# Kernel tuning notes

Measured on AMD Instinct MI355X. Metric: run time of the kernel, lower is better.

## Reference

```python
import jax, jax.numpy as jnp
import numpy as np

ALPHA = 0.2  # LeakyReLU negative slope


def setup_inputs() -> dict:
    key = jax.random.key(0)
    k1, k2, k3 = jax.random.split(key, 3)
    B, N, IN, OUT = 64, 2048, 1024, 1024
    features = jax.random.normal(k1, (B, N, IN), dtype=jnp.float32)
    # Xavier-uniform-ish scaling for weights
    W = jax.random.normal(k2, (OUT, IN), dtype=jnp.float32) * (1.0 / np.sqrt(IN))
    w_b = jnp.zeros((OUT,), dtype=jnp.float32)
    a_w = jax.random.normal(k3, (2 * OUT,), dtype=jnp.float32) * (1.0 / np.sqrt(2 * OUT))
    a_b = jnp.zeros((), dtype=jnp.float32)
    bias_out = jnp.zeros((OUT,), dtype=jnp.float32)
    return {"features": features, "W": W, "w_b": w_b, "a_w": a_w, "a_b": a_b, "bias_out": bias_out}


def reference(features, W, w_b, a_w, a_b, bias_out):
    # h = Linear(in_dim, out_dim)(features): [B, N, D]
    h = jnp.einsum('bni,di->bnd', features, W) + w_b
    D = h.shape[-1]
    a1, a2 = a_w[:D], a_w[D:]
    # concat([h_expand, h]) @ a == h[:, :1] . a1 + h . a2  (h_expand broadcasts node 0)
    e = (h[:, 0:1, :] @ a1[:, None]) + jnp.einsum('bnd,d->bn', h, a2)[..., None] + a_b  # [B, N, 1]
    e = jnp.where(e >= 0, e, ALPHA * e)  # LeakyReLU
    attention = jax.nn.softmax(e, axis=1)  # softmax over nodes, [B, N, 1]
    # dropout p=0.0 -> identity
    pooled = jnp.einsum('bnk,bnd->bkd', attention, h)  # [B, 1, D]
    return jax.nn.relu(pooled + bias_out)
```

## Files before the change

kernel.cpp:

```cpp
#include <hip/hip_runtime.h>

#define ALPHA 0.2f
constexpr int B_   = 64;
constexpr int N_   = 2048;
constexpr int IN_  = 1024;
constexpr int OUT_ = 1024;
constexpr int CHUNK = 256;
constexpr int NCH   = N_ / CHUNK;
constexpr int RPW   = CHUNK / 4;

constexpr size_t WA2   = 0;
constexpr size_t E0P   = 1024;
constexpr size_t ZPART = 5120;
constexpr size_t GPART = 8192;
constexpr size_t GV    = 532480;

__device__ inline float wave_reduce_sum(float v) {
    #pragma unroll
    for (int off = 32; off > 0; off >>= 1) v += __shfl_xor(v, off);
    return v;
}

__global__ void kPre(const float* __restrict__ W, const float* __restrict__ f,
                     const float* __restrict__ wb, const float* __restrict__ aw,
                     float* __restrict__ ws) {
    int s = blockIdx.x;
    int t = threadIdx.x;
    int c  = t & 15;
    int rg = t >> 4;
    int col = s * 16 + c;
    float a1acc = 0.f, a2acc = 0.f;
    for (int i = 0; i < 64; ++i) {
        int d = rg * 64 + i;
        float w = W[(size_t)d * IN_ + col];
        a1acc += aw[d] * w;
        a2acc += aw[OUT_ + d] * w;
    }
    __shared__ float s1[16][16], s2[16][16];
    __shared__ float wa1L[16];
    __shared__ float wbshare_s;
    s1[rg][c] = a1acc;
    s2[rg][c] = a2acc;
    __syncthreads();
    if (t < 16) {
        float x1 = 0.f, x2 = 0.f;
        #pragma unroll
        for (int r = 0; r < 16; ++r) { x1 += s1[r][t]; x2 += s2[r][t]; }
        wa1L[t] = x1;
        ws[WA2 + s * 16 + t] = x2;
    }
    if (t == 0) {
        float x = 0.f;
        #pragma unroll
        for (int c2 = 0; c2 < 16; ++c2) {
            int cc = s * 16 + c2;
            x += wb[cc] * (aw[cc] + aw[OUT_ + cc]);
        }
        wbshare_s = x;
    }
    __syncthreads();
    int b = t >> 2, q = t & 3;
    float4 fv = ((const float4*)(f + (size_t)b * N_ * IN_ + s * 16))[q];
    float4 w1 = ((const float4*)wa1L)[q];
    float dotv = fv.x * w1.x + fv.y * w1.y + fv.z * w1.z + fv.w * w1.w;
    dotv += __shfl_xor(dotv, 1);
    dotv += __shfl_xor(dotv, 2);
    if (q == 0) ws[E0P + s * 64 + b] = dotv + wbshare_s;
}

__global__ void kMain(const float* __restrict__ f, const float* __restrict__ ab,
                      float* __restrict__ ws) {
    int b = blockIdx.y, chunk = blockIdx.x;
    int t = threadIdx.x, wave = t >> 6, lane = t & 63;

    __shared__ float cstS;
    if (t < 64) {
        float v = ws[E0P + (size_t)t * 64 + b];
        v = wave_reduce_sum(v);
        if (t == 0) cstS = v + ab[0];
    }
    __syncthreads();
    float cst = cstS;

    const float4* wa2_4 = (const float4*)(ws + WA2);
    float4 ra2[4];
    #pragma unroll
    for (int k = 0; k < 4; ++k) ra2[k] = wa2_4[k * 64 + lane];

    const float4* fbase = (const float4*)(f + ((size_t)b * N_ + (size_t)chunk * CHUNK) * IN_);
    float4 acc[4];
    #pragma unroll
    for (int k = 0; k < 4; ++k) acc[k] = make_float4(0.f, 0.f, 0.f, 0.f);
    float z = 0.f;

    float4 v[4], nv[4];
    int r = wave;
    #pragma unroll
    for (int k = 0; k < 4; ++k) v[k] = fbase[(size_t)r * 256 + k * 64 + lane];

    for (int i = 0; i < RPW; ++i) {
        int rn = r + 4;
        if (i + 1 < RPW) {
            #pragma unroll
            for (int k = 0; k < 4; ++k) nv[k] = fbase[(size_t)rn * 256 + k * 64 + lane];
        }
        float dot = 0.f;
        #pragma unroll
        for (int k = 0; k < 4; ++k)
            dot += v[k].x * ra2[k].x + v[k].y * ra2[k].y + v[k].z * ra2[k].z + v[k].w * ra2[k].w;
        dot = wave_reduce_sum(dot);
        float e = dot + cst;
        e = e >= 0.f ? e : ALPHA * e;
        float w = __expf(e);
        z += w;
        #pragma unroll
        for (int k = 0; k < 4; ++k) {
            acc[k].x += w * v[k].x; acc[k].y += w * v[k].y;
            acc[k].z += w * v[k].z; acc[k].w += w * v[k].w;
        }
        if (i + 1 < RPW) {
            #pragma unroll
            for (int k = 0; k < 4; ++k) v[k] = nv[k];
        }
        r = rn;
    }

    __shared__ float4 gbuf[4][256];
    __shared__ float  zbuf[4];
    #pragma unroll
    for (int k = 0; k < 4; ++k) gbuf[wave][k * 64 + lane] = acc[k];
    if (lane == 0) zbuf[wave] = z;
    __syncthreads();
    float4 s0 = gbuf[0][t], s1 = gbuf[1][t], s2 = gbuf[2][t], s3 = gbuf[3][t];
    float4 s = make_float4(s0.x + s1.x + s2.x + s3.x, s0.y + s1.y + s2.y + s3.y,
                           s0.z + s1.z + s2.z + s3.z, s0.w + s1.w + s2.w + s3.w);
    ((float4*)(ws + GPART))[((size_t)b * NCH + chunk) * 256 + t] = s;
    if (t == 0) ws[ZPART + b * NCH + chunk] = zbuf[0] + zbuf[1] + zbuf[2] + zbuf[3];
}

__global__ void kE(float* __restrict__ ws) {
    int b = blockIdx.x, t = threadIdx.x;
    __shared__ float zinv;
    if (t == 0) {
        float zz = 0.f;
        #pragma unroll
        for (int c = 0; c < NCH; ++c) zz += ws[ZPART + b * NCH + c];
        zinv = 1.0f / zz;
    }
    __syncthreads();
    const float4* gp = (const float4*)(ws + GPART);
    float4 acc = make_float4(0.f, 0.f, 0.f, 0.f);
    #pragma unroll
    for (int c = 0; c < NCH; ++c) {
        float4 v = gp[((size_t)b * NCH + c) * 256 + t];
        acc.x += v.x; acc.y += v.y; acc.z += v.z; acc.w += v.w;
    }
    acc.x *= zinv; acc.y *= zinv; acc.z *= zinv; acc.w *= zinv;
    ((float4*)(ws + GV))[b * 256 + t] = acc;
}

__global__ void kF(const float* __restrict__ W, const float* __restrict__ wb,
                   const float* __restrict__ bias, const float* __restrict__ ws,
                   float* __restrict__ out) {
    int t = threadIdx.x, wave = t >> 6, lane = t & 63;
    int d  = blockIdx.x * 4 + wave;
    int b0 = blockIdx.y * 32;
    const float4* w4 = (const float4*)(W + (size_t)d * IN_);
    float4 wreg[4];
    #pragma unroll
    for (int k = 0; k < 4; ++k) wreg[k] = w4[k * 64 + lane];
    float wbb = wb[d] + bias[d];
    const float4* gv = (const float4*)(ws + GV);
    #pragma unroll 4
    for (int bi = 0; bi < 32; ++bi) {
        int b = b0 + bi;
        float acc = 0.f;
        #pragma unroll
        for (int k = 0; k < 4; ++k) {
            float4 g = gv[b * 256 + k * 64 + lane];
            acc += g.x * wreg[k].x + g.y * wreg[k].y + g.z * wreg[k].z + g.w * wreg[k].w;
        }
        acc = wave_reduce_sum(acc);
        if (lane == 0) {
            float p = acc + wbb;
            out[(size_t)b * OUT_ + d] = p > 0.f ? p : 0.f;
        }
    }
}

extern "C" void kernel_launch(void* const* d_in, const int* in_sizes, int n_in,
                              void* d_out, int out_size, void* d_ws, size_t ws_size,
                              hipStream_t stream) {
    const float* f    = (const float*)d_in[0];
    const float* W    = (const float*)d_in[1];
    const float* wb   = (const float*)d_in[2];
    const float* aw   = (const float*)d_in[3];
    const float* ab   = (const float*)d_in[4];
    const float* bias = (const float*)d_in[5];
    float* out = (float*)d_out;
    float* ws  = (float*)d_ws;

    kPre <<<dim3(64), 256, 0, stream>>>(W, f, wb, aw, ws);
    kMain<<<dim3(NCH, B_), 256, 0, stream>>>(f, ab, ws);
    kE   <<<dim3(B_), 256, 0, stream>>>(ws);
    kF   <<<dim3(OUT_ / 4, 2), 256, 0, stream>>>(W, wb, bias, ws, out);
}
```

Before: 122.3 us.

## Fuse four kernels into one cooperative kernel with grid-wide syncs

Merges the precompute, main attention-pooling, reduction and output projection kernels into a single cooperative kernel of 512 blocks separated by grid.sync barriers. This is meant to remove the launch overhead and inter-kernel gaps of four separate launches. In exchange the grid is fixed at 512 blocks and depends on all of them being co-resident, and each grid.sync adds its own barrier cost. Several phases also leave most blocks idle.

```diff
diff --git a/kernel.cpp b/kernel.cpp
--- a/kernel.cpp
+++ b/kernel.cpp
@@ -1,4 +1,7 @@
 #include <hip/hip_runtime.h>
+#include <hip/hip_cooperative_groups.h>
+
+namespace cg = cooperative_groups;
 
 #define ALPHA 0.2f
 constexpr int B_   = 64;
@@ -8,6 +11,7 @@
 constexpr int CHUNK = 256;
 constexpr int NCH   = N_ / CHUNK;
 constexpr int RPW   = CHUNK / 4;
+constexpr int GRID  = 512;
 
 constexpr size_t WA2   = 0;
 constexpr size_t E0P   = 1024;
@@ -21,169 +25,176 @@
     return v;
 }
 
-__global__ void kPre(const float* __restrict__ W, const float* __restrict__ f,
-                     const float* __restrict__ wb, const float* __restrict__ aw,
-                     float* __restrict__ ws) {
-    int s = blockIdx.x;
-    int t = threadIdx.x;
-    int c  = t & 15;
-    int rg = t >> 4;
-    int col = s * 16 + c;
-    float a1acc = 0.f, a2acc = 0.f;
-    for (int i = 0; i < 64; ++i) {
-        int d = rg * 64 + i;
-        float w = W[(size_t)d * IN_ + col];
-        a1acc += aw[d] * w;
-        a2acc += aw[OUT_ + d] * w;
-    }
-    __shared__ float s1[16][16], s2[16][16];
-    __shared__ float wa1L[16];
-    __shared__ float wbshare_s;
-    s1[rg][c] = a1acc;
-    s2[rg][c] = a2acc;
-    __syncthreads();
-    if (t < 16) {
-        float x1 = 0.f, x2 = 0.f;
-        #pragma unroll
-        for (int r = 0; r < 16; ++r) { x1 += s1[r][t]; x2 += s2[r][t]; }
-        wa1L[t] = x1;
-        ws[WA2 + s * 16 + t] = x2;
-    }
-    if (t == 0) {
-        float x = 0.f;
-        #pragma unroll
-        for (int c2 = 0; c2 < 16; ++c2) {
-            int cc = s * 16 + c2;
-            x += wb[cc] * (aw[cc] + aw[OUT_ + cc]);
-        }
-        wbshare_s = x;
-    }
-    __syncthreads();
-    int b = t >> 2, q = t & 3;
-    float4 fv = ((const float4*)(f + (size_t)b * N_ * IN_ + s * 16))[q];
-    float4 w1 = ((const float4*)wa1L)[q];
-    float dotv = fv.x * w1.x + fv.y * w1.y + fv.z * w1.z + fv.w * w1.w;
-    dotv += __shfl_xor(dotv, 1);
-    dotv += __shfl_xor(dotv, 2);
-    if (q == 0) ws[E0P + s * 64 + b] = dotv + wbshare_s;
-}
-
-__global__ void kMain(const float* __restrict__ f, const float* __restrict__ ab,
-                      float* __restrict__ ws) {
-    int b = blockIdx.y, chunk = blockIdx.x;
-    int t = threadIdx.x, wave = t >> 6, lane = t & 63;
-
-    __shared__ float cstS;
-    if (t < 64) {
-        float v = ws[E0P + (size_t)t * 64 + b];
-        v = wave_reduce_sum(v);
-        if (t == 0) cstS = v + ab[0];
-    }
-    __syncthreads();
-    float cst = cstS;
-
-    const float4* wa2_4 = (const float4*)(ws + WA2);
-    float4 ra2[4];
-    #pragma unroll
-    for (int k = 0; k < 4; ++k) ra2[k] = wa2_4[k * 64 + lane];
-
-    const float4* fbase = (const float4*)(f + ((size_t)b * N_ + (size_t)chunk * CHUNK) * IN_);
-    float4 acc[4];
-    #pragma unroll
-    for (int k = 0; k < 4; ++k) acc[k] = make_float4(0.f, 0.f, 0.f, 0.f);
-    float z = 0.f;
-
-    float4 v[4], nv[4];
-    int r = wave;
-    #pragma unroll
-    for (int k = 0; k < 4; ++k) v[k] = fbase[(size_t)r * 256 + k * 64 + lane];
-
-    for (int i = 0; i < RPW; ++i) {
-        int rn = r + 4;
-        if (i + 1 < RPW) {
-            #pragma unroll
-            for (int k = 0; k < 4; ++k) nv[k] = fbase[(size_t)rn * 256 + k * 64 + lane];
-        }
-        float dot = 0.f;
-        #pragma unroll
-        for (int k = 0; k < 4; ++k)
-            dot += v[k].x * ra2[k].x + v[k].y * ra2[k].y + v[k].z * ra2[k].z + v[k].w * ra2[k].w;
-        dot = wave_reduce_sum(dot);
-        float e = dot + cst;
-        e = e >= 0.f ? e : ALPHA * e;
-        float w = __expf(e);
-        z += w;
-        #pragma unroll
-        for (int k = 0; k < 4; ++k) {
-            acc[k].x += w * v[k].x; acc[k].y += w * v[k].y;
-            acc[k].z += w * v[k].z; acc[k].w += w * v[k].w;
-        }
-        if (i + 1 < RPW) {
-            #pragma unroll
-            for (int k = 0; k < 4; ++k) v[k] = nv[k];
-        }
-        r = rn;
-    }
+__global__ void __launch_bounds__(256, 2)
+kAll(const float* __restrict__ W, const float* __restrict__ f,
+     const float* __restrict__ wb, const float* __restrict__ aw,
+     const float* __restrict__ ab, const float* __restrict__ bias,
+     float* __restrict__ out, float* __restrict__ ws) {
+    cg::grid_group grid = cg::this_grid();
+    const int bid = blockIdx.x;
+    const int t = threadIdx.x;
+    const int wave = t >> 6, lane = t & 63;
 
     __shared__ float4 gbuf[4][256];
     __shared__ float  zbuf[4];
-    #pragma unroll
-    for (int k = 0; k < 4; ++k) gbuf[wave][k * 64 + lane] = acc[k];
-    if (lane == 0) zbuf[wave] = z;
-    __syncthreads();
-    float4 s0 = gbuf[0][t], s1 = gbuf[1][t], s2 = gbuf[2][t], s3 = gbuf[3][t];
-    float4 s = make_float4(s0.x + s1.x + s2.x + s3.x, s0.y + s1.y + s2.y + s3.y,
-                           s0.z + s1.z + s2.z + s3.z, s0.w + s1.w + s2.w + s3.w);
-    ((float4*)(ws + GPART))[((size_t)b * NCH + chunk) * 256 + t] = s;
-    if (t == 0) ws[ZPART + b * NCH + chunk] = zbuf[0] + zbuf[1] + zbuf[2] + zbuf[3];
-}
-
-__global__ void kE(float* __restrict__ ws) {
-    int b = blockIdx.x, t = threadIdx.x;
-    __shared__ float zinv;
-    if (t == 0) {
-        float zz = 0.f;
-        #pragma unroll
-        for (int c = 0; c < NCH; ++c) zz += ws[ZPART + b * NCH + c];
-        zinv = 1.0f / zz;
-    }
-    __syncthreads();
-    const float4* gp = (const float4*)(ws + GPART);
-    float4 acc = make_float4(0.f, 0.f, 0.f, 0.f);
-    #pragma unroll
-    for (int c = 0; c < NCH; ++c) {
-        float4 v = gp[((size_t)b * NCH + c) * 256 + t];
-        acc.x += v.x; acc.y += v.y; acc.z += v.z; acc.w += v.w;
-    }
-    acc.x *= zinv; acc.y *= zinv; acc.z *= zinv; acc.w *= zinv;
-    ((float4*)(ws + GV))[b * 256 + t] = acc;
-}
-
-__global__ void kF(const float* __restrict__ W, const float* __restrict__ wb,
-                   const float* __restrict__ bias, const float* __restrict__ ws,
-                   float* __restrict__ out) {
-    int t = threadIdx.x, wave = t >> 6, lane = t & 63;
-    int d  = blockIdx.x * 4 + wave;
-    int b0 = blockIdx.y * 32;
-    const float4* w4 = (const float4*)(W + (size_t)d * IN_);
-    float4 wreg[4];
-    #pragma unroll
-    for (int k = 0; k < 4; ++k) wreg[k] = w4[k * 64 + lane];
-    float wbb = wb[d] + bias[d];
-    const float4* gv = (const float4*)(ws + GV);
-    #pragma unroll 4
-    for (int bi = 0; bi < 32; ++bi) {
-        int b = b0 + bi;
-        float acc = 0.f;
-        #pragma unroll
-        for (int k = 0; k < 4; ++k) {
-            float4 g = gv[b * 256 + k * 64 + lane];
-            acc += g.x * wreg[k].x + g.y * wreg[k].y + g.z * wreg[k].z + g.w * wreg[k].w;
-        }
-        acc = wave_reduce_sum(acc);
-        if (lane == 0) {
-            float p = acc + wbb;
-            out[(size_t)b * OUT_ + d] = p > 0.f ? p : 0.f;
+    __shared__ float  s1[16][16], s2[16][16];
+    __shared__ float  wa1L[16];
+    __shared__ float  wbshare_s;
+    __shared__ float  cstS;
+    __shared__ float  zinv;
+
+    if (bid < 64) {
+        int s = bid;
+        int c  = t & 15;
+        int rg = t >> 4;
+        int col = s * 16 + c;
+        float a1acc = 0.f, a2acc = 0.f;
+        for (int i = 0; i < 64; ++i) {
+            int d = rg * 64 + i;
+            float w = W[(size_t)d * IN_ + col];
+            a1acc += aw[d] * w;
+            a2acc += aw[OUT_ + d] * w;
+        }
+        s1[rg][c] = a1acc;
+        s2[rg][c] = a2acc;
+        __syncthreads();
+        if (t < 16) {
+            float x1 = 0.f, x2 = 0.f;
+            #pragma unroll
+            for (int r = 0; r < 16; ++r) { x1 += s1[r][t]; x2 += s2[r][t]; }
+            wa1L[t] = x1;
+            ws[WA2 + s * 16 + t] = x2;
+        }
+        if (t == 0) {
+            float x = 0.f;
+            #pragma unroll
+            for (int c2 = 0; c2 < 16; ++c2) {
+                int cc = s * 16 + c2;
+                x += wb[cc] * (aw[cc] + aw[OUT_ + cc]);
+            }
+            wbshare_s = x;
+        }
+        __syncthreads();
+        int b = t >> 2, q = t & 3;
+        float4 fv = ((const float4*)(f + (size_t)b * N_ * IN_ + s * 16))[q];
+        float4 w1 = ((const float4*)wa1L)[q];
+        float dotv = fv.x * w1.x + fv.y * w1.y + fv.z * w1.z + fv.w * w1.w;
+        dotv += __shfl_xor(dotv, 1);
+        dotv += __shfl_xor(dotv, 2);
+        if (q == 0) ws[E0P + s * 64 + b] = dotv + wbshare_s;
+    }
+    grid.sync();
+
+    {
+        int b = bid >> 3, chunk = bid & 7;
+
+        if (t < 64) {
+            float v = ws[E0P + (size_t)t * 64 + b];
+            v = wave_reduce_sum(v);
+            if (t == 0) cstS = v + ab[0];
+        }
+        __syncthreads();
+        float cst = cstS;
+
+        const float4* wa2_4 = (const float4*)(ws + WA2);
+        float4 ra2[4];
+        #pragma unroll
+        for (int k = 0; k < 4; ++k) ra2[k] = wa2_4[k * 64 + lane];
+
+        const float4* fbase = (const float4*)(f + ((size_t)b * N_ + (size_t)chunk * CHUNK) * IN_);
+        float4 acc[4];
+        #pragma unroll
+        for (int k = 0; k < 4; ++k) acc[k] = make_float4(0.f, 0.f, 0.f, 0.f);
+        float z = 0.f;
+
+        float4 v[4], nv[4];
+        int r = wave;
+        #pragma unroll
+        for (int k = 0; k < 4; ++k) v[k] = fbase[(size_t)r * 256 + k * 64 + lane];
+
+        for (int i = 0; i < RPW; ++i) {
+            int rn = r + 4;
+            if (i + 1 < RPW) {
+                #pragma unroll
+                for (int k = 0; k < 4; ++k) nv[k] = fbase[(size_t)rn * 256 + k * 64 + lane];
+            }
+            float dot = 0.f;
+            #pragma unroll
+            for (int k = 0; k < 4; ++k)
+                dot += v[k].x * ra2[k].x + v[k].y * ra2[k].y + v[k].z * ra2[k].z + v[k].w * ra2[k].w;
+            dot = wave_reduce_sum(dot);
+            float e = dot + cst;
+            e = e >= 0.f ? e : ALPHA * e;
+            float w = __expf(e);
+            z += w;
+            #pragma unroll
+            for (int k = 0; k < 4; ++k) {
+                acc[k].x += w * v[k].x; acc[k].y += w * v[k].y;
+                acc[k].z += w * v[k].z; acc[k].w += w * v[k].w;
+            }
+            if (i + 1 < RPW) {
+                #pragma unroll
+                for (int k = 0; k < 4; ++k) v[k] = nv[k];
+            }
+            r = rn;
+        }
+
+        #pragma unroll
+        for (int k = 0; k < 4; ++k) gbuf[wave][k * 64 + lane] = acc[k];
+        if (lane == 0) zbuf[wave] = z;
+        __syncthreads();
+        float4 p0 = gbuf[0][t], p1 = gbuf[1][t], p2 = gbuf[2][t], p3 = gbuf[3][t];
+        float4 s = make_float4(p0.x + p1.x + p2.x + p3.x, p0.y + p1.y + p2.y + p3.y,
+                               p0.z + p1.z + p2.z + p3.z, p0.w + p1.w + p2.w + p3.w);
+        ((float4*)(ws + GPART))[((size_t)b * NCH + chunk) * 256 + t] = s;
+        if (t == 0) ws[ZPART + b * NCH + chunk] = zbuf[0] + zbuf[1] + zbuf[2] + zbuf[3];
+    }
+    grid.sync();
+
+    if (bid < 64) {
+        int b = bid;
+        if (t == 0) {
+            float zz = 0.f;
+            #pragma unroll
+            for (int c = 0; c < NCH; ++c) zz += ws[ZPART + b * NCH + c];
+            zinv = 1.0f / zz;
+        }
+        __syncthreads();
+        const float4* gp = (const float4*)(ws + GPART);
+        float4 acc = make_float4(0.f, 0.f, 0.f, 0.f);
+        #pragma unroll
+        for (int c = 0; c < NCH; ++c) {
+            float4 v = gp[((size_t)b * NCH + c) * 256 + t];
+            acc.x += v.x; acc.y += v.y; acc.z += v.z; acc.w += v.w;
+        }
+        acc.x *= zinv; acc.y *= zinv; acc.z *= zinv; acc.w *= zinv;
+        ((float4*)(ws + GV))[b * 256 + t] = acc;
+    }
+    grid.sync();
+
+    {
+        int d  = (bid & 255) * 4 + wave;
+        int b0 = (bid >> 8) * 32;
+        const float4* w4 = (const float4*)(W + (size_t)d * IN_);
+        float4 wreg[4];
+        #pragma unroll
+        for (int k = 0; k < 4; ++k) wreg[k] = w4[k * 64 + lane];
+        float wbb = wb[d] + bias[d];
+        const float4* gv = (const float4*)(ws + GV);
+        #pragma unroll 4
+        for (int bi = 0; bi < 32; ++bi) {
+            int b = b0 + bi;
+            float acc = 0.f;
+            #pragma unroll
+            for (int k = 0; k < 4; ++k) {
+                float4 g = gv[b * 256 + k * 64 + lane];
+                acc += g.x * wreg[k].x + g.y * wreg[k].y + g.z * wreg[k].z + g.w * wreg[k].w;
+            }
+            acc = wave_reduce_sum(acc);
+            if (lane == 0) {
+                float p = acc + wbb;
+                out[(size_t)b * OUT_ + d] = p > 0.f ? p : 0.f;
+            }
         }
     }
 }
@@ -200,8 +211,8 @@
     float* out = (float*)d_out;
     float* ws  = (float*)d_ws;
 
-    kPre <<<dim3(64), 256, 0, stream>>>(W, f, wb, aw, ws);
-    kMain<<<dim3(NCH, B_), 256, 0, stream>>>(f, ab, ws);
-    kE   <<<dim3(B_), 256, 0, stream>>>(ws);
-    kF   <<<dim3(OUT_ / 4, 2), 256, 0, stream>>>(W, wb, bias, ws, out);
+    void* args[] = { (void*)&W, (void*)&f, (void*)&wb, (void*)&aw,
+                     (void*)&ab, (void*)&bias, (void*)&out, (void*)&ws };
+    hipLaunchCooperativeKernel((const void*)kAll, dim3(GRID), dim3(256),
+                               args, 0, stream);
 }
```

Result: slower. 296.2 us (+142.3%).
